# Kernel tuning notes

Measured on AMD Instinct MI355X. Metric: run time of the kernel, lower is better.

The kernel has to match this reference:

```python
import jax, jax.numpy as jnp
from jax import lax
import numpy as np

WIN = 11
SIGMA = 1.5
PAD = WIN // 2
C1 = 0.01 ** 2
C2 = 0.03 ** 2


def _gauss1d():
    x = jnp.arange(WIN, dtype=jnp.float32) - (WIN // 2)
    k = jnp.exp(-(x ** 2) / (2.0 * SIGMA ** 2))
    return k / k.sum()


def _blur3d(x, k1d):
    # Separable 3D gaussian blur (mathematically identical to the outer-product
    # 3D kernel used by the torch module, since kernel3d = k1d (x) k1d (x) k1d).
    # x: [B, 1, D, H, W]
    dn = ('NCDHW', 'OIDHW', 'NCDHW')
    x = lax.conv_general_dilated(x, k1d.reshape(1, 1, WIN, 1, 1), (1, 1, 1),
                                 [(PAD, PAD), (0, 0), (0, 0)], dimension_numbers=dn)
    x = lax.conv_general_dilated(x, k1d.reshape(1, 1, 1, WIN, 1), (1, 1, 1),
                                 [(0, 0), (PAD, PAD), (0, 0)], dimension_numbers=dn)
    x = lax.conv_general_dilated(x, k1d.reshape(1, 1, 1, 1, WIN), (1, 1, 1),
                                 [(0, 0), (0, 0), (PAD, PAD)], dimension_numbers=dn)
    return x


def setup_inputs() -> dict:
    key = jax.random.key(0)
    k1, k2 = jax.random.split(key)
    shape = (2, 1, 192, 192, 192)
    img1 = jax.random.uniform(k1, shape, dtype=jnp.float32)
    img2 = jax.random.uniform(k2, shape, dtype=jnp.float32)
    return {"img1": img1, "img2": img2}


def reference(img1, img2):
    k1d = _gauss1d().astype(img1.dtype)
    mu1 = _blur3d(img1, k1d)
    mu2 = _blur3d(img2, k1d)
    mu1_sq = mu1 * mu1
    mu2_sq = mu2 * mu2
    mu1mu2 = mu1 * mu2
    sigma1 = _blur3d(img1 * img1, k1d) - mu1_sq
    sigma2 = _blur3d(img2 * img2, k1d) - mu2_sq
    sigma12 = _blur3d(img1 * img2, k1d) - mu1mu2
    num = (2.0 * mu1mu2 + C1) * (2.0 * sigma12 + C2)
    den = (mu1_sq + mu2_sq + C1) * (sigma1 + sigma2 + C2)
    ssim_map = num / den
    return ssim_map.mean()  # size_average=True
```

## Files before the change

kernel.cpp:

```cpp
#include <hip/hip_runtime.h>

#define NB 2
#define DD 192
#define HH 192
#define WW 192
#define HWSZ (HH * WW)
#define C1F 0.0001f
#define C2F 0.0009f

#define TH 16
#define TW 32
#define CHUNK 32
#define TSTEPS (CHUNK + 10)
#define NCH (DD / CHUNK)
#define NTH (HH / TH)
#define NTW (WW / TW)
#define NBLK (NB * NCH * NTH * NTW)

#define SROWS (TH + 10)
#define SCOLS 42
#define SP2 44
#define TQ 36
#define NSTG (SROWS * SCOLS)
#define NWT (SROWS * (TW / 4))

#define KWLIST { 0.00102838f, 0.00759876f, 0.03600077f, 0.10936071f, 0.21300556f, \
                 0.26601172f, 0.21300556f, 0.10936071f, 0.03600077f, 0.00759876f, 0.00102838f }

__device__ __forceinline__ float ssim_val(float mu1, float mu2, float A, float Bm) {
  const float mu1sq = mu1 * mu1, mu2sq = mu2 * mu2, mu12 = mu1 * mu2;
  const float num = (2.f * mu12 + C1F) * (0.5f * (A - Bm) - 2.f * mu12 + C2F);
  const float den = (mu1sq + mu2sq + C1F) * (0.5f * (A + Bm) - mu1sq - mu2sq + C2F);
  return num * __builtin_amdgcn_rcpf(den);
}

__global__ __launch_bounds__(256) void ssim_fused(
    const float* __restrict__ x, const float* __restrict__ y,
    float* __restrict__ partials) {
  const float KW[11] = KWLIST;

  int bid = blockIdx.x;
  const int tw = bid % NTW; bid /= NTW;
  const int th = bid % NTH; bid /= NTH;
  const int c  = bid % NCH; bid /= NCH;
  const int b  = bid;
  const int h0 = th * TH, w0 = tw * TW, c0 = c * CHUNK;

  __shared__ __align__(16) float2 s2[SROWS][SP2];
  __shared__ float4 t4[SROWS][TQ];

  const int tid = threadIdx.x;
  const int cl  = tid & 31;
  const int rg  = tid >> 5;
  const int r0  = 2 * rg;
  const int clp2 = (cl & ~3) | (((cl & 3) + (cl >> 2)) & 3);

  int  sIdx[5], sOff[5];
  bool sOk[5];
#pragma unroll
  for (int k = 0; k < 5; ++k) {
    const int q = tid + 256 * k;
    const bool act = (q < NSTG);
    const int row = q / SCOLS, col = q % SCOLS;
    const int gh = h0 - 5 + row, gw = w0 - 5 + col;
    sOk[k]  = act && (unsigned)gh < (unsigned)HH && (unsigned)gw < (unsigned)WW;
    sIdx[k] = row * SP2 + col;
    sOff[k] = gh * WW + gw;
  }
  const bool wAct = (tid < NWT);
  const int  wr = tid >> 3;
  const int  wq = tid & 7;
  const int  tBase = wr * TQ + 4 * wq;
  const int  st0 = tBase + ((0 + wq) & 3);
  const int  st1 = tBase + ((1 + wq) & 3);
  const int  st2 = tBase + ((2 + wq) & 3);
  const int  st3 = tBase + ((3 + wq) & 3);

  {
    const float2 z = make_float2(0.f, 0.f);
    for (int q = tid; q < SROWS * SP2; q += 256) (&s2[0][0])[q] = z;
  }
  __syncthreads();

  const float* xb = x + (size_t)b * DD * HWSZ;
  const float* yb = y + (size_t)b * DD * HWSZ;

  float pend0[4][11], pend1[4][11];
#pragma unroll
  for (int f = 0; f < 4; ++f)
#pragma unroll
    for (int i = 0; i < 11; ++i) { pend0[f][i] = 0.f; pend1[f][i] = 0.f; }

  float px[5], py[5];
#pragma unroll
  for (int k = 0; k < 5; ++k) { px[k] = 0.f; py[k] = 0.f; }

  if (c0 >= 5) {
    const float* xs = xb + (size_t)(c0 - 5) * HWSZ;
    const float* ys = yb + (size_t)(c0 - 5) * HWSZ;
#pragma unroll
    for (int k = 0; k < 5; ++k)
      if (sOk[k]) { px[k] = xs[sOff[k]]; py[k] = ys[sOff[k]]; }
  }

  float lsum = 0.f;
  int p = 0;

  for (int t = 0; t < TSTEPS; ++t) {
    const int d = c0 - 5 + t;
    const bool dv = (d >= 0) && (d < DD);

    if (dv) {
#pragma unroll
      for (int k = 0; k < 5; ++k)
        if (sOk[k]) (&s2[0][0])[sIdx[k]] = make_float2(px[k], py[k]);
    }
    {
      const int dn = d + 1;
      if ((t + 1) < TSTEPS && dn >= 0 && dn < DD) {
        const float* xs = xb + (size_t)dn * HWSZ;
        const float* ys = yb + (size_t)dn * HWSZ;
#pragma unroll
        for (int k = 0; k < 5; ++k)
          if (sOk[k]) { px[k] = xs[sOff[k]]; py[k] = ys[sOff[k]]; }
      }
    }

    float4 B0 = make_float4(0.f, 0.f, 0.f, 0.f);
    float4 B1 = B0;

    if (dv) {
      __syncthreads();
      if (wAct) {
        const float4* srow4 = (const float4*)&s2[wr][0];
        float4 a0 = make_float4(0.f, 0.f, 0.f, 0.f), a1 = a0, a2 = a0, a3 = a0;
#pragma unroll
        for (int u2 = 0; u2 < 7; ++u2) {
          const float4 v2 = srow4[2 * wq + u2];
#pragma unroll
          for (int h = 0; h < 2; ++h) {
            const int   u  = 2 * u2 + h;
            const float xx = h ? v2.z : v2.x;
            const float yy = h ? v2.w : v2.y;
            const float sm = xx + yy, df = xx - yy;
            const float s2q = sm * sm, d2q = df * df;
            if (u <= 10)           { const float k = KW[u];     a0.x += k*xx; a0.y += k*yy; a0.z += k*s2q; a0.w += k*d2q; }
            if (u >= 1 && u <= 11) { const float k = KW[u - 1]; a1.x += k*xx; a1.y += k*yy; a1.z += k*s2q; a1.w += k*d2q; }
            if (u >= 2 && u <= 12) { const float k = KW[u - 2]; a2.x += k*xx; a2.y += k*yy; a2.z += k*s2q; a2.w += k*d2q; }
            if (u >= 3)            { const float k = KW[u - 3]; a3.x += k*xx; a3.y += k*yy; a3.z += k*s2q; a3.w += k*d2q; }
          }
        }
        float4* tb = &t4[0][0];
        tb[st0] = a0; tb[st1] = a1; tb[st2] = a2; tb[st3] = a3;
      }
      __syncthreads();

#pragma unroll
      for (int u = 0; u < 12; ++u) {
        const float4 v = t4[r0 + u][clp2];
        if (u <= 10) { const float k = KW[u];     B0.x += k*v.x; B0.y += k*v.y; B0.z += k*v.z; B0.w += k*v.w; }
        if (u >= 1)  { const float k = KW[u - 1]; B1.x += k*v.x; B1.y += k*v.y; B1.z += k*v.z; B1.w += k*v.w; }
      }
    }

#define RING_CASE(P)                                                        \
    case P: {                                                               \
      if (dv) {                                                             \
        _Pragma("unroll")                                                   \
        for (int kk = 0; kk < 11; ++kk) {                                   \
          const int   sl = (P + 1 + kk) % 11;                               \
          const float wg = KW[kk];                                          \
          pend0[0][sl] += wg * B0.x; pend0[1][sl] += wg * B0.y;             \
          pend0[2][sl] += wg * B0.z; pend0[3][sl] += wg * B0.w;             \
          pend1[0][sl] += wg * B1.x; pend1[1][sl] += wg * B1.y;             \
          pend1[2][sl] += wg * B1.z; pend1[3][sl] += wg * B1.w;             \
        }                                                                   \
      }                                                                     \
      const int sc = (P + 1) % 11;                                          \
      if (t >= 10) {                                                        \
        lsum += ssim_val(pend0[0][sc], pend0[1][sc], pend0[2][sc], pend0[3][sc]); \
        lsum += ssim_val(pend1[0][sc], pend1[1][sc], pend1[2][sc], pend1[3][sc]); \
      }                                                                     \
      pend0[0][sc] = 0.f; pend0[1][sc] = 0.f;                               \
      pend0[2][sc] = 0.f; pend0[3][sc] = 0.f;                               \
      pend1[0][sc] = 0.f; pend1[1][sc] = 0.f;                               \
      pend1[2][sc] = 0.f; pend1[3][sc] = 0.f;                               \
    } break;

    switch (p) {
      RING_CASE(0) RING_CASE(1) RING_CASE(2) RING_CASE(3) RING_CASE(4)
      RING_CASE(5) RING_CASE(6) RING_CASE(7) RING_CASE(8) RING_CASE(9)
      RING_CASE(10)
    }
#undef RING_CASE
    p = (p + 1 == 11) ? 0 : p + 1;
  }

  for (int off = 32; off > 0; off >>= 1) lsum += __shfl_down(lsum, off, 64);
  __shared__ float wsum[4];
  if ((tid & 63) == 0) wsum[tid >> 6] = lsum;
  __syncthreads();
  if (tid == 0) partials[blockIdx.x] = wsum[0] + wsum[1] + wsum[2] + wsum[3];
}

__global__ __launch_bounds__(256) void ssim_reduce(
    const float* __restrict__ partials, float* __restrict__ out) {
  __shared__ double sd[256];
  double a = 0.0;
  for (int i = threadIdx.x; i < NBLK; i += 256) a += (double)partials[i];
  sd[threadIdx.x] = a;
  __syncthreads();
  for (int s = 128; s > 0; s >>= 1) {
    if ((int)threadIdx.x < s) sd[threadIdx.x] += sd[threadIdx.x + s];
    __syncthreads();
  }
  if (threadIdx.x == 0) {
    out[0] = (float)(sd[0] / (double)((size_t)NB * DD * HH * WW));
  }
}

extern "C" void kernel_launch(void* const* d_in, const int* in_sizes, int n_in,
                              void* d_out, int out_size, void* d_ws, size_t ws_size,
                              hipStream_t stream) {
  const float* img1 = (const float*)d_in[0];
  const float* img2 = (const float*)d_in[1];
  float* out = (float*)d_out;
  float* partials = (float*)d_ws;

  ssim_fused<<<NBLK, 256, 0, stream>>>(img1, img2, partials);
  ssim_reduce<<<1, 256, 0, stream>>>(partials, out);
}
```

Measured before the change: 171.9 us.

## Double-buffer staging, use packed FMA, and grow tile to 32 rows with 512 threads

Doubles the H tile and block size to 512 threads, which cuts halo overhead per output. Adds a double-buffered shared staging plane with a two-deep register prefetch so global loads overlap the W-blur. Replaces the scalar FMAs in all three blur passes with v_pk_fma_f32 on float2 pairs. The trade-offs are higher register pressure from the 512-thread launch bound and the packed ring buffers, an extra barrier per step, and fewer total blocks.

```diff
diff --git a/kernel.cpp b/kernel.cpp
--- a/kernel.cpp
+++ b/kernel.cpp
@@ -8,7 +8,7 @@
 #define C1F 0.0001f
 #define C2F 0.0009f
 
-#define TH 16
+#define TH 32
 #define TW 32
 #define CHUNK 32
 #define TSTEPS (CHUNK + 10)
@@ -16,16 +16,21 @@
 #define NTH (HH / TH)
 #define NTW (WW / TW)
 #define NBLK (NB * NCH * NTH * NTW)
+#define NTHR 512
 
 #define SROWS (TH + 10)
 #define SCOLS 42
-#define SP2 44
-#define TQ 36
+#define SP2 50
+#define TQ 33
 #define NSTG (SROWS * SCOLS)
 #define NWT (SROWS * (TW / 4))
 
 #define KWLIST { 0.00102838f, 0.00759876f, 0.03600077f, 0.10936071f, 0.21300556f, \
                  0.26601172f, 0.21300556f, 0.10936071f, 0.03600077f, 0.00759876f, 0.00102838f }
+
+__device__ __forceinline__ void pk_fma(float2& acc, float2 a, float2 k2) {
+  asm("v_pk_fma_f32 %0, %1, %2, %0" : "+v"(acc) : "v"(a), "v"(k2));
+}
 
 __device__ __forceinline__ float ssim_val(float mu1, float mu2, float A, float Bm) {
   const float mu1sq = mu1 * mu1, mu2sq = mu2 * mu2, mu12 = mu1 * mu2;
@@ -34,10 +39,13 @@
   return num * __builtin_amdgcn_rcpf(den);
 }
 
-__global__ __launch_bounds__(256) void ssim_fused(
+__global__ __launch_bounds__(NTHR) void ssim_fused(
     const float* __restrict__ x, const float* __restrict__ y,
     float* __restrict__ partials) {
   const float KW[11] = KWLIST;
+  float2 KW2[11];
+#pragma unroll
+  for (int i = 0; i < 11; ++i) KW2[i] = make_float2(KW[i], KW[i]);
 
   int bid = blockIdx.x;
   const int tw = bid % NTW; bid /= NTW;
@@ -46,7 +54,7 @@
   const int b  = bid;
   const int h0 = th * TH, w0 = tw * TW, c0 = c * CHUNK;
 
-  __shared__ __align__(16) float2 s2[SROWS][SP2];
+  __shared__ __align__(16) float2 s2[2][SROWS][SP2];
   __shared__ float4 t4[SROWS][TQ];
 
   const int tid = threadIdx.x;
@@ -55,11 +63,11 @@
   const int r0  = 2 * rg;
   const int clp2 = (cl & ~3) | (((cl & 3) + (cl >> 2)) & 3);
 
-  int  sIdx[5], sOff[5];
-  bool sOk[5];
-#pragma unroll
-  for (int k = 0; k < 5; ++k) {
-    const int q = tid + 256 * k;
+  int  sIdx[4], sOff[4];
+  bool sOk[4];
+#pragma unroll
+  for (int k = 0; k < 4; ++k) {
+    const int q = tid + NTHR * k;
     const bool act = (q < NSTG);
     const int row = q / SCOLS, col = q % SCOLS;
     const int gh = h0 - 5 + row, gw = w0 - 5 + col;
@@ -78,88 +86,94 @@
 
   {
     const float2 z = make_float2(0.f, 0.f);
-    for (int q = tid; q < SROWS * SP2; q += 256) (&s2[0][0])[q] = z;
-  }
-  __syncthreads();
+    float2* sb = &s2[0][0][0];
+    for (int q = tid; q < 2 * SROWS * SP2; q += NTHR) sb[q] = z;
+  }
 
   const float* xb = x + (size_t)b * DD * HWSZ;
   const float* yb = y + (size_t)b * DD * HWSZ;
 
-  float pend0[4][11], pend1[4][11];
-#pragma unroll
-  for (int f = 0; f < 4; ++f)
-#pragma unroll
-    for (int i = 0; i < 11; ++i) { pend0[f][i] = 0.f; pend1[f][i] = 0.f; }
-
-  float px[5], py[5];
-#pragma unroll
-  for (int k = 0; k < 5; ++k) { px[k] = 0.f; py[k] = 0.f; }
-
-  if (c0 >= 5) {
-    const float* xs = xb + (size_t)(c0 - 5) * HWSZ;
-    const float* ys = yb + (size_t)(c0 - 5) * HWSZ;
-#pragma unroll
-    for (int k = 0; k < 5; ++k)
+  float px[4], py[4];
+#pragma unroll
+  for (int k = 0; k < 4; ++k) { px[k] = 0.f; py[k] = 0.f; }
+
+  auto do_prefetch = [&](int g) {
+    const float* xs = xb + (size_t)g * HWSZ;
+    const float* ys = yb + (size_t)g * HWSZ;
+#pragma unroll
+    for (int k = 0; k < 4; ++k)
       if (sOk[k]) { px[k] = xs[sOff[k]]; py[k] = ys[sOff[k]]; }
+  };
+  auto do_stage = [&](float2* s2buf) {
+#pragma unroll
+    for (int k = 0; k < 4; ++k)
+      if (sOk[k]) s2buf[sIdx[k]] = make_float2(px[k], py[k]);
+  };
+  auto do_wblur = [&](const float2* s2buf) {
+    if (wAct) {
+      const float4* srow4 = (const float4*)(s2buf + wr * SP2);
+      float2 a0p = make_float2(0.f, 0.f), a0q = a0p, a1p = a0p, a1q = a0p,
+             a2p = a0p, a2q = a0p, a3p = a0p, a3q = a0p;
+#pragma unroll
+      for (int u2 = 0; u2 < 7; ++u2) {
+        const float4 v2 = srow4[2 * wq + u2];
+#pragma unroll
+        for (int h = 0; h < 2; ++h) {
+          const int    u  = 2 * u2 + h;
+          const float  xx = h ? v2.z : v2.x;
+          const float  yy = h ? v2.w : v2.y;
+          const float2 xy = make_float2(xx, yy);
+          const float  sm = xx + yy, df = xx - yy;
+          const float2 sqdq = make_float2(sm * sm, df * df);
+          if (u <= 10)           { pk_fma(a0p, xy, KW2[u]);     pk_fma(a0q, sqdq, KW2[u]); }
+          if (u >= 1 && u <= 11) { pk_fma(a1p, xy, KW2[u - 1]); pk_fma(a1q, sqdq, KW2[u - 1]); }
+          if (u >= 2 && u <= 12) { pk_fma(a2p, xy, KW2[u - 2]); pk_fma(a2q, sqdq, KW2[u - 2]); }
+          if (u >= 3)            { pk_fma(a3p, xy, KW2[u - 3]); pk_fma(a3q, sqdq, KW2[u - 3]); }
+        }
+      }
+      float4* tb = &t4[0][0];
+      tb[st0] = make_float4(a0p.x, a0p.y, a0q.x, a0q.y);
+      tb[st1] = make_float4(a1p.x, a1p.y, a1q.x, a1q.y);
+      tb[st2] = make_float4(a2p.x, a2p.y, a2q.x, a2q.y);
+      tb[st3] = make_float4(a3p.x, a3p.y, a3q.x, a3q.y);
+    }
+  };
+
+  float2 p0a[11], p0b[11], p1a[11], p1b[11];
+#pragma unroll
+  for (int i = 0; i < 11; ++i) {
+    p0a[i] = make_float2(0.f, 0.f); p0b[i] = p0a[i];
+    p1a[i] = p0a[i]; p1b[i] = p0a[i];
   }
 
   float lsum = 0.f;
+
+  __syncthreads();
+  if (c0 - 5 >= 0) { do_prefetch(c0 - 5); do_stage(&s2[0][0][0]); }
+  if (c0 - 4 >= 0) do_prefetch(c0 - 4);
+  __syncthreads();
+
   int p = 0;
-
   for (int t = 0; t < TSTEPS; ++t) {
+    const int cur = t & 1, nxt = cur ^ 1;
     const int d = c0 - 5 + t;
     const bool dv = (d >= 0) && (d < DD);
 
+    if (dv) do_wblur(&s2[cur][0][0]);
+    if ((t + 1) < TSTEPS && (d + 1) >= 0 && (d + 1) < DD) do_stage(&s2[nxt][0][0]);
+    if ((t + 2) < TSTEPS && (d + 2) >= 0 && (d + 2) < DD) do_prefetch(d + 2);
+    __syncthreads();
+
+    float2 B0a = make_float2(0.f, 0.f), B0b = B0a, B1a = B0a, B1b = B0a;
     if (dv) {
-#pragma unroll
-      for (int k = 0; k < 5; ++k)
-        if (sOk[k]) (&s2[0][0])[sIdx[k]] = make_float2(px[k], py[k]);
-    }
-    {
-      const int dn = d + 1;
-      if ((t + 1) < TSTEPS && dn >= 0 && dn < DD) {
-        const float* xs = xb + (size_t)dn * HWSZ;
-        const float* ys = yb + (size_t)dn * HWSZ;
-#pragma unroll
-        for (int k = 0; k < 5; ++k)
-          if (sOk[k]) { px[k] = xs[sOff[k]]; py[k] = ys[sOff[k]]; }
-      }
-    }
-
-    float4 B0 = make_float4(0.f, 0.f, 0.f, 0.f);
-    float4 B1 = B0;
-
-    if (dv) {
-      __syncthreads();
-      if (wAct) {
-        const float4* srow4 = (const float4*)&s2[wr][0];
-        float4 a0 = make_float4(0.f, 0.f, 0.f, 0.f), a1 = a0, a2 = a0, a3 = a0;
-#pragma unroll
-        for (int u2 = 0; u2 < 7; ++u2) {
-          const float4 v2 = srow4[2 * wq + u2];
-#pragma unroll
-          for (int h = 0; h < 2; ++h) {
-            const int   u  = 2 * u2 + h;
-            const float xx = h ? v2.z : v2.x;
-            const float yy = h ? v2.w : v2.y;
-            const float sm = xx + yy, df = xx - yy;
-            const float s2q = sm * sm, d2q = df * df;
-            if (u <= 10)           { const float k = KW[u];     a0.x += k*xx; a0.y += k*yy; a0.z += k*s2q; a0.w += k*d2q; }
-            if (u >= 1 && u <= 11) { const float k = KW[u - 1]; a1.x += k*xx; a1.y += k*yy; a1.z += k*s2q; a1.w += k*d2q; }
-            if (u >= 2 && u <= 12) { const float k = KW[u - 2]; a2.x += k*xx; a2.y += k*yy; a2.z += k*s2q; a2.w += k*d2q; }
-            if (u >= 3)            { const float k = KW[u - 3]; a3.x += k*xx; a3.y += k*yy; a3.z += k*s2q; a3.w += k*d2q; }
-          }
-        }
-        float4* tb = &t4[0][0];
-        tb[st0] = a0; tb[st1] = a1; tb[st2] = a2; tb[st3] = a3;
-      }
-      __syncthreads();
-
+      const float4* tb = &t4[0][0];
 #pragma unroll
       for (int u = 0; u < 12; ++u) {
-        const float4 v = t4[r0 + u][clp2];
-        if (u <= 10) { const float k = KW[u];     B0.x += k*v.x; B0.y += k*v.y; B0.z += k*v.z; B0.w += k*v.w; }
-        if (u >= 1)  { const float k = KW[u - 1]; B1.x += k*v.x; B1.y += k*v.y; B1.z += k*v.z; B1.w += k*v.w; }
+        const float4 v = tb[(r0 + u) * TQ + clp2];
+        const float2 vxy = make_float2(v.x, v.y);
+        const float2 vzw = make_float2(v.z, v.w);
+        if (u <= 10) { pk_fma(B0a, vxy, KW2[u]);     pk_fma(B0b, vzw, KW2[u]); }
+        if (u >= 1)  { pk_fma(B1a, vxy, KW2[u - 1]); pk_fma(B1b, vzw, KW2[u - 1]); }
       }
     }
 
@@ -168,23 +182,18 @@
       if (dv) {                                                             \
         _Pragma("unroll")                                                   \
         for (int kk = 0; kk < 11; ++kk) {                                   \
-          const int   sl = (P + 1 + kk) % 11;                               \
-          const float wg = KW[kk];                                          \
-          pend0[0][sl] += wg * B0.x; pend0[1][sl] += wg * B0.y;             \
-          pend0[2][sl] += wg * B0.z; pend0[3][sl] += wg * B0.w;             \
-          pend1[0][sl] += wg * B1.x; pend1[1][sl] += wg * B1.y;             \
-          pend1[2][sl] += wg * B1.z; pend1[3][sl] += wg * B1.w;             \
+          const int sl = (P + 1 + kk) % 11;                                 \
+          pk_fma(p0a[sl], B0a, KW2[kk]); pk_fma(p0b[sl], B0b, KW2[kk]);     \
+          pk_fma(p1a[sl], B1a, KW2[kk]); pk_fma(p1b[sl], B1b, KW2[kk]);     \
         }                                                                   \
       }                                                                     \
       const int sc = (P + 1) % 11;                                          \
       if (t >= 10) {                                                        \
-        lsum += ssim_val(pend0[0][sc], pend0[1][sc], pend0[2][sc], pend0[3][sc]); \
-        lsum += ssim_val(pend1[0][sc], pend1[1][sc], pend1[2][sc], pend1[3][sc]); \
+        lsum += ssim_val(p0a[sc].x, p0a[sc].y, p0b[sc].x, p0b[sc].y);       \
+        lsum += ssim_val(p1a[sc].x, p1a[sc].y, p1b[sc].x, p1b[sc].y);       \
       }                                                                     \
-      pend0[0][sc] = 0.f; pend0[1][sc] = 0.f;                               \
-      pend0[2][sc] = 0.f; pend0[3][sc] = 0.f;                               \
-      pend1[0][sc] = 0.f; pend1[1][sc] = 0.f;                               \
-      pend1[2][sc] = 0.f; pend1[3][sc] = 0.f;                               \
+      p0a[sc] = make_float2(0.f, 0.f); p0b[sc] = make_float2(0.f, 0.f);     \
+      p1a[sc] = make_float2(0.f, 0.f); p1b[sc] = make_float2(0.f, 0.f);     \
     } break;
 
     switch (p) {
@@ -194,13 +203,20 @@
     }
 #undef RING_CASE
     p = (p + 1 == 11) ? 0 : p + 1;
+
+    __syncthreads();
   }
 
   for (int off = 32; off > 0; off >>= 1) lsum += __shfl_down(lsum, off, 64);
-  __shared__ float wsum[4];
+  __shared__ float wsum[8];
   if ((tid & 63) == 0) wsum[tid >> 6] = lsum;
   __syncthreads();
-  if (tid == 0) partials[blockIdx.x] = wsum[0] + wsum[1] + wsum[2] + wsum[3];
+  if (tid == 0) {
+    float s = 0.f;
+#pragma unroll
+    for (int i = 0; i < 8; ++i) s += wsum[i];
+    partials[blockIdx.x] = s;
+  }
 }
 
 __global__ __launch_bounds__(256) void ssim_reduce(
@@ -227,6 +243,6 @@
   float* out = (float*)d_out;
   float* partials = (float*)d_ws;
 
-  ssim_fused<<<NBLK, 256, 0, stream>>>(img1, img2, partials);
+  ssim_fused<<<NBLK, NTHR, 0, stream>>>(img1, img2, partials);
   ssim_reduce<<<1, 256, 0, stream>>>(partials, out);
 }
```

After: 221.3 us. +28.7%, slower.
